# Kernel tuning notes

Hardware: AMD Instinct MI355X
Metric: run time of the kernel (lower is better)

## Reference

```python
import jax, jax.numpy as jnp
import numpy as np

IMG_H = 224
P = 3                      # roi_output_size
FEAT_HW = 13               # alexnet features[:7] spatial size for 224 input
SCALE = FEAT_HW / IMG_H
C_FEAT = 384
N_VIS = C_FEAT * P * P     # 3456
HID = 300
N_CLASSES = 4
BN_EPS = 1e-5
B, N, K2 = 8, 1024, 10     # images, total boxes, 2*context_size


def _conv(x, w, b, stride, pad):
    y = jax.lax.conv_general_dilated(x, w, (stride, stride), [(pad, pad), (pad, pad)],
                                     dimension_numbers=('NCHW', 'OIHW', 'NCHW'))
    return y + b[None, :, None, None]


def _maxpool3s2(x):
    return jax.lax.reduce_window(x, -jnp.inf, jax.lax.max, (1, 1, 3, 3), (1, 1, 2, 2), 'VALID')


def alexnet_feat(x, c1w, c1b, c2w, c2b, c3w, c3b):
    # torchvision alexnet features[:7] -> ends at conv3, NO trailing ReLU
    x = jax.nn.relu(_conv(x, c1w, c1b, 4, 2))
    x = _maxpool3s2(x)
    x = jax.nn.relu(_conv(x, c2w, c2b, 1, 2))
    x = _maxpool3s2(x)
    return _conv(x, c3w, c3b, 1, 1)


def roi_pool(feat, bboxes):
    # torchvision RoIPool: round coords by scale, per-bin max, empty bin -> 0
    H, W = feat.shape[2], feat.shape[3]
    img = bboxes[:, 0].astype(jnp.int32)
    c = jnp.round(bboxes[:, 1:] * SCALE).astype(jnp.int32)  # x1,y1,x2,y2 on feature grid
    x1, y1, x2, y2 = c[:, 0], c[:, 1], c[:, 2], c[:, 3]
    roi_w = jnp.maximum(x2 - x1 + 1, 1)
    roi_h = jnp.maximum(y2 - y1 + 1, 1)
    f = feat[img]                                   # [N,C,H,W] gather per roi
    hs = jnp.arange(H)
    ws = jnp.arange(W)
    bins = []
    for ph in range(P):
        hstart = jnp.clip(y1 + (ph * roi_h) // P, 0, H)
        hend = jnp.clip(y1 + ((ph + 1) * roi_h + P - 1) // P, 0, H)  # ceil
        mh = (hs[None, :] >= hstart[:, None]) & (hs[None, :] < hend[:, None])  # [N,H]
        for pw in range(P):
            wstart = jnp.clip(x1 + (pw * roi_w) // P, 0, W)
            wend = jnp.clip(x1 + ((pw + 1) * roi_w + P - 1) // P, 0, W)
            mw = (ws[None, :] >= wstart[:, None]) & (ws[None, :] < wend[:, None])
            mask = (mh[:, :, None] & mw[:, None, :])[:, None, :, :]  # [N,1,H,W]
            v = jnp.where(mask, f, -jnp.inf).max(axis=(2, 3))         # [N,C]
            empty = (hend <= hstart) | (wend <= wstart)
            bins.append(jnp.where(empty[:, None], 0.0, v))
    # bins ordered (ph,pw) -> [N,C,P,P], flatten like torch .view(N,-1)
    return jnp.stack(bins, axis=-1).reshape(-1, C_FEAT * P * P)


def _bn(x, g, b, m, v):
    return (x - m) * (g * jax.lax.rsqrt(v + BN_EPS)) + b


def _encoder(x, w1, b1, g, be, m, v, w2, b2):
    h = jax.nn.relu(_bn(x @ w1 + b1, g, be, m, v))  # dropout = identity (eval)
    return h @ w2 + b2


def setup_inputs() -> dict:
    key = jax.random.key(0)
    ks = jax.random.split(key, 24)
    images = jax.random.uniform(ks[0], (B, 3, IMG_H, IMG_H), jnp.float32)
    img_idx = jax.random.randint(ks[1], (N,), 0, B).astype(jnp.float32)
    xy = jax.random.uniform(ks[2], (N, 2), jnp.float32, 0.0, IMG_H - 48.0)
    wh = jax.random.uniform(ks[3], (N, 2), jnp.float32, 8.0, 48.0)
    bboxes = jnp.concatenate([img_idx[:, None], xy, xy + wh], axis=1)
    context_indices = jax.random.randint(ks[4], (N, K2), -1, N)  # -1 = padding -> zero row

    def w(k, shape, fan_in):
        return jax.random.normal(k, shape, jnp.float32) * (1.0 / np.sqrt(fan_in))

    n_total = N_VIS + HID + 4
    return {
        'images': images, 'bboxes': bboxes, 'context_indices': context_indices,
        'c1w': w(ks[5], (64, 3, 11, 11), 3 * 121), 'c1b': jnp.zeros((64,)),
        'c2w': w(ks[6], (192, 64, 5, 5), 64 * 25), 'c2b': jnp.zeros((192,)),
        'c3w': w(ks[7], (384, 192, 3, 3), 192 * 9), 'c3b': jnp.zeros((384,)),
        'enc_w1': w(ks[8], (N_VIS, HID), N_VIS), 'enc_b1': jnp.zeros((HID,)),
        'enc_g': jnp.ones((HID,)), 'enc_be': jnp.zeros((HID,)),
        'enc_m': jax.random.normal(ks[9], (HID,)) * 0.1,
        'enc_v': jax.random.uniform(ks[10], (HID,), jnp.float32, 0.5, 1.5),
        'enc_w2': w(ks[11], (HID, HID), HID), 'enc_b2': jnp.zeros((HID,)),
        'att_w': w(ks[12], (2 * HID, 1), 2 * HID), 'att_b': jnp.zeros((1,)),
        'dec_w1': w(ks[13], (n_total, n_total), n_total), 'dec_b1': jnp.zeros((n_total,)),
        'dec_g': jnp.ones((n_total,)), 'dec_be': jnp.zeros((n_total,)),
        'dec_m': jax.random.normal(ks[14], (n_total,)) * 0.1,
        'dec_v': jax.random.uniform(ks[15], (n_total,), jnp.float32, 0.5, 1.5),
        'dec_w2': w(ks[16], (n_total, N_CLASSES), n_total), 'dec_b2': jnp.zeros((N_CLASSES,)),
    }


def reference(images, bboxes, context_indices, c1w, c1b, c2w, c2b, c3w, c3b,
              enc_w1, enc_b1, enc_g, enc_be, enc_m, enc_v, enc_w2, enc_b2,
              att_w, att_b, dec_w1, dec_b1, dec_g, dec_be, dec_m, dec_v, dec_w2, dec_b2):
    n = bboxes.shape[0]
    k2 = context_indices.shape[1]
    conv_feat = alexnet_feat(images, c1w, c1b, c2w, c2b, c3w, c3b)      # [B,384,13,13]
    own = roi_pool(conv_feat, bboxes)                                   # [n, 3456]
    padded = jnp.concatenate([own, jnp.zeros((1, N_VIS), own.dtype)], 0)
    ctx = padded[context_indices.reshape(-1)].reshape(n, k2, N_VIS)     # -1 wraps to zero row

    own_enc = _encoder(own, enc_w1, enc_b1, enc_g, enc_be, enc_m, enc_v, enc_w2, enc_b2)
    ctx_enc = _encoder(ctx.reshape(n * k2, N_VIS), enc_w1, enc_b1, enc_g, enc_be,
                       enc_m, enc_v, enc_w2, enc_b2).reshape(n, k2, HID)
    # attention_layer(concat(own_enc, ctx_enc)) split into the two halves of att_w
    scores = (own_enc @ att_w[:HID, 0])[:, None] + ctx_enc @ att_w[HID:, 0] + att_b[0]  # [n,k2]
    wts = jax.nn.softmax(scores, axis=1)
    ctx_rep = jnp.einsum('nk,nkh->nh', wts, ctx_enc)                    # [n, HID]

    xywh = jnp.concatenate([bboxes[:, 1:3], bboxes[:, 3:5] - bboxes[:, 1:3]], axis=1)
    combined = jnp.concatenate([own, ctx_rep, xywh], axis=1)            # [n, 3760]
    h = jax.nn.relu(_bn(combined @ dec_w1 + dec_b1, dec_g, dec_be, dec_m, dec_v))
    return h @ dec_w2 + dec_b2                                          # [n, n_classes]
```

## Files before the change

### kernel.cpp

```cpp
#include <hip/hip_runtime.h>
#include <hip/hip_bf16.h>
#include <math.h>

#define C_FEAT 384
#define N_VIS (C_FEAT * 9)
#define HID 300
#define BN_EPS 1e-5f
#define BATCH 8
#define NROI 1024
#define K2 10
#define NTOT (N_VIS + HID + 4)
#define KPAD_DEC 3776
#define KPAD_ENC2 320

typedef _Float16 f16;
typedef f16 f16x8 __attribute__((ext_vector_type(8)));
typedef float f32x4 __attribute__((ext_vector_type(4)));
typedef int i32x4 __attribute__((ext_vector_type(4)));

__global__ void split_rowmajor(const float* __restrict__ in, f16* __restrict__ oh,
                               f16* __restrict__ ol, int R, int C, int Cpad)
{
    int idx = blockIdx.x * blockDim.x + threadIdx.x;
    if (idx >= R * Cpad) return;
    int r = idx / Cpad, c = idx % Cpad;
    float v = (c < C) ? in[(size_t)r * C + c] : 0.f;
    f16 h = (f16)v;
    oh[idx] = h;
    ol[idx] = (f16)(v - (float)h);
}

__global__ void convert_rowmajor(const float* __restrict__ in, f16* __restrict__ oh,
                                 int R, int C, int Cpad)
{
    int idx = blockIdx.x * blockDim.x + threadIdx.x;
    if (idx >= R * Cpad) return;
    int r = idx / Cpad, c = idx % Cpad;
    float v = (c < C) ? in[(size_t)r * C + c] : 0.f;
    oh[idx] = (f16)v;
}

__global__ void transpose_split(const float* __restrict__ W, int K, int Ntot, int nc0, int NC,
                                int Kpad, f16* __restrict__ Bh, f16* __restrict__ Bl)
{
    __shared__ float T[32][33];
    int k0 = blockIdx.x * 32, n0 = blockIdx.y * 32;
    int tc = threadIdx.x & 31, tr = threadIdx.x >> 5;
    #pragma unroll
    for (int i = 0; i < 4; ++i) {
        int r = tr + i * 8;
        int gk = k0 + r, nloc = n0 + tc, gn = nc0 + nloc;
        float v = 0.f;
        if (gk < K && nloc < NC && gn < Ntot) v = W[(size_t)gk * Ntot + gn];
        T[r][tc] = v;
    }
    __syncthreads();
    #pragma unroll
    for (int i = 0; i < 4; ++i) {
        int nr = tr + i * 8;
        int n = n0 + nr;
        if (n >= NC) continue;
        float v = T[tc][nr];
        f16 h = (f16)v;
        size_t o = (size_t)n * Kpad + k0 + tc;
        Bh[o] = h;
        Bl[o] = (f16)(v - (float)h);
    }
}

__global__ void transpose_convert(const float* __restrict__ W, int K, int Ntot, int nc0, int NC,
                                  int Kpad, f16* __restrict__ Bh)
{
    __shared__ float T[32][33];
    int k0 = blockIdx.x * 32, n0 = blockIdx.y * 32;
    int tc = threadIdx.x & 31, tr = threadIdx.x >> 5;
    #pragma unroll
    for (int i = 0; i < 4; ++i) {
        int r = tr + i * 8;
        int gk = k0 + r, nloc = n0 + tc, gn = nc0 + nloc;
        float v = 0.f;
        if (gk < K && nloc < NC && gn < Ntot) v = W[(size_t)gk * Ntot + gn];
        T[r][tc] = v;
    }
    __syncthreads();
    #pragma unroll
    for (int i = 0; i < 4; ++i) {
        int nr = tr + i * 8;
        int n = n0 + nr;
        if (n >= NC) continue;
        Bh[(size_t)n * Kpad + k0 + tc] = (f16)T[tc][nr];
    }
}

__global__ void im2col1_f16(const float* __restrict__ img, f16* __restrict__ ch, int b0, int nb)
{
    int idx = blockIdx.x * blockDim.x + threadIdx.x;
    int total = nb * 3025 * 384;
    if (idx >= total) return;
    int k = idx % 384, r = idx / 384;
    int ow = r % 55, t = r / 55;
    int oh = t % 55, bi = t / 55;
    float v = 0.f;
    if (k < 363) {
        int ic = k / 121, q = k % 121;
        int kh = q / 11, kw = q % 11;
        int ih = oh * 4 - 2 + kh, iw = ow * 4 - 2 + kw;
        if (ih >= 0 && ih < 224 && iw >= 0 && iw < 224)
            v = img[(((size_t)(b0 + bi) * 3 + ic) * 224 + ih) * 224 + iw];
    }
    ch[idx] = (f16)v;
}

__global__ void im2col2_f16(const float* __restrict__ in, f16* __restrict__ ch, int b0, int nb)
{
    int idx = blockIdx.x * blockDim.x + threadIdx.x;
    int total = nb * 729 * 1600;
    if (idx >= total) return;
    int k = idx % 1600, r = idx / 1600;
    int ow = r % 27, t = r / 27;
    int oh = t % 27, bi = t / 27;
    int ic = k / 25, q = k % 25;
    int kh = q / 5, kw = q % 5;
    int ih = oh - 2 + kh, iw = ow - 2 + kw;
    float v = 0.f;
    if (ih >= 0 && ih < 27 && iw >= 0 && iw < 27)
        v = in[(((size_t)(b0 + bi) * 27 + ih) * 27 + iw) * 64 + ic];
    ch[idx] = (f16)v;
}

__global__ void im2col3_f16(const float* __restrict__ in, f16* __restrict__ ch)
{
    int idx = blockIdx.x * blockDim.x + threadIdx.x;
    int total = 8 * 169 * 1728;
    if (idx >= total) return;
    int k = idx % 1728, r = idx / 1728;
    int ow = r % 13, t = r / 13;
    int oh = t % 13, bi = t / 13;
    int ic = k / 9, q = k % 9;
    int kh = q / 3, kw = q % 3;
    int ih = oh - 1 + kh, iw = ow - 1 + kw;
    float v = 0.f;
    if (ih >= 0 && ih < 13 && iw >= 0 && iw < 13)
        v = in[(((size_t)bi * 13 + ih) * 13 + iw) * 192 + ic];
    ch[idx] = (f16)v;
}

#define LDH 40
template<int TM, int TN, int BS, int MODE, int SWZ, int SPLITK, int PASSES>
__global__ __launch_bounds__(BS) void gemm_f16x3(
    const f16* __restrict__ Ah, const f16* __restrict__ Al, int lda,
    const f16* __restrict__ Bh, const f16* __restrict__ Bl, int ldb,
    float* __restrict__ C, int ldc, int M, int N, int K,
    const float* __restrict__ bias, const float* __restrict__ g,
    const float* __restrict__ be, const float* __restrict__ mean,
    const float* __restrict__ var)
{
    constexpr int NW = BS / 64;
    constexpr int WROWS = NW / 2;
    constexpr int WM = TM / (16 * WROWS);
    constexpr int WN = TN / 32;
    constexpr int AV = TM * 4 / BS;
    constexpr int BV = TN * 4 / BS;
    constexpr bool P3 = (PASSES == 3);
    __shared__ f16 sAh[TM * LDH], sBh[TN * LDH];
    __shared__ f16 sAl[(P3 ? TM : 1) * LDH], sBl[(P3 ? TN : 1) * LDH];
    int tid = threadIdx.x;
    int lane = tid & 63, w = tid >> 6;
    int wr = w >> 1, wc = w & 1;

    int bm, bn;
    if (SWZ == 2) {
        int bid = blockIdx.x;
        int x = bid & 7, l = bid >> 3;
        int mt = 2 * (x >> 1) + l / 15;
        int nt = 15 * (x & 1) + l % 15;
        bm = mt * TM; bn = nt * TN;
    } else {
        bm = blockIdx.y * TM;
        bn = blockIdx.x * TN;
    }

    int ksBeg = 0, ksEnd = K;
    if (SPLITK > 1) {
        int kc = K / SPLITK;
        ksBeg = blockIdx.z * kc;
        ksEnd = (blockIdx.z == SPLITK - 1) ? K : ksBeg + kc;
    }

    f32x4 acc[WM][WN];
    #pragma unroll
    for (int i = 0; i < WM; ++i)
        #pragma unroll
        for (int j = 0; j < WN; ++j) acc[i][j] = (f32x4){0.f, 0.f, 0.f, 0.f};

    const f16* pAh[AV]; const f16* pAl[AV]; int abase[AV]; bool avld[AV];
    #pragma unroll
    for (int i = 0; i < AV; ++i) {
        int seg = tid * AV + i;
        int row = seg >> 2, ko = (seg & 3) * 8;
        int gr = bm + row;
        avld[i] = gr < M;
        pAh[i] = Ah + (size_t)(avld[i] ? gr : 0) * lda + ko;
        if (P3) pAl[i] = Al + (size_t)(avld[i] ? gr : 0) * lda + ko;
        abase[i] = row * LDH + ko;
    }
    const f16* pBh[BV]; const f16* pBl[BV]; int bbase[BV]; bool bvld[BV];
    #pragma unroll
    for (int i = 0; i < BV; ++i) {
        int seg = tid * BV + i;
        int row = seg >> 2, ko = (seg & 3) * 8;
        int gr = bn + row;
        bvld[i] = gr < N;
        pBh[i] = Bh + (size_t)(bvld[i] ? gr : 0) * ldb + ko;
        if (P3) pBl[i] = Bl + (size_t)(bvld[i] ? gr : 0) * ldb + ko;
        bbase[i] = row * LDH + ko;
    }

    const i32x4 zz = {0, 0, 0, 0};
    i32x4 rAh[AV], rAl[AV], rBh[BV], rBl[BV];

    auto load_step = [&](int k0) {
        #pragma unroll
        for (int i = 0; i < AV; ++i) {
            rAh[i] = avld[i] ? *(const i32x4*)(pAh[i] + k0) : zz;
            if (P3) rAl[i] = avld[i] ? *(const i32x4*)(pAl[i] + k0) : zz;
        }
        #pragma unroll
        for (int i = 0; i < BV; ++i) {
            rBh[i] = bvld[i] ? *(const i32x4*)(pBh[i] + k0) : zz;
            if (P3) rBl[i] = bvld[i] ? *(const i32x4*)(pBl[i] + k0) : zz;
        }
    };
    load_step(ksBeg);

    int kfo = (lane >> 4) * 8;
    int rr = lane & 15;

    for (int k0 = ksBeg; k0 < ksEnd; k0 += 32) {
        __syncthreads();
        #pragma unroll
        for (int i = 0; i < AV; ++i) {
            *(i32x4*)&sAh[abase[i]] = rAh[i];
            if (P3) *(i32x4*)&sAl[abase[i]] = rAl[i];
        }
        #pragma unroll
        for (int i = 0; i < BV; ++i) {
            *(i32x4*)&sBh[bbase[i]] = rBh[i];
            if (P3) *(i32x4*)&sBl[bbase[i]] = rBl[i];
        }
        __syncthreads();
        if (k0 + 32 < ksEnd) load_step(k0 + 32);

        f16x8 fah[WM], fal[WM], fbh[WN], fbl[WN];
        #pragma unroll
        for (int m = 0; m < WM; ++m) {
            int row = wr * (WM * 16) + m * 16 + rr;
            fah[m] = *(const f16x8*)&sAh[row * LDH + kfo];
            if (P3) fal[m] = *(const f16x8*)&sAl[row * LDH + kfo];
        }
        #pragma unroll
        for (int n = 0; n < WN; ++n) {
            int row = wc * (WN * 16) + n * 16 + rr;
            fbh[n] = *(const f16x8*)&sBh[row * LDH + kfo];
            if (P3) fbl[n] = *(const f16x8*)&sBl[row * LDH + kfo];
        }
        #pragma unroll
        for (int m = 0; m < WM; ++m)
            #pragma unroll
            for (int n = 0; n < WN; ++n) {
                acc[m][n] = __builtin_amdgcn_mfma_f32_16x16x32_f16(fah[m], fbh[n], acc[m][n], 0, 0, 0);
                if (P3) {
                    acc[m][n] = __builtin_amdgcn_mfma_f32_16x16x32_f16(fah[m], fbl[n], acc[m][n], 0, 0, 0);
                    acc[m][n] = __builtin_amdgcn_mfma_f32_16x16x32_f16(fal[m], fbh[n], acc[m][n], 0, 0, 0);
                }
            }
    }

    int crl = lane >> 4;
    size_t zoff = (SPLITK > 1) ? (size_t)blockIdx.z * M : 0;
    #pragma unroll
    for (int m = 0; m < WM; ++m) {
        #pragma unroll
        for (int n = 0; n < WN; ++n) {
            int gn = bn + wc * (WN * 16) + n * 16 + rr;
            if (gn >= N) continue;
            #pragma unroll
            for (int r = 0; r < 4; ++r) {
                int gm = bm + wr * (WM * 16) + m * 16 + crl * 4 + r;
                if (gm >= M) continue;
                if (SPLITK > 1) {
                    C[(zoff + gm) * ldc + gn] = acc[m][n][r];
                } else {
                    float v = acc[m][n][r] + bias[gn];
                    if (MODE == 1) {
                        float s = g[gn] / sqrtf(var[gn] + BN_EPS);
                        v = (v - mean[gn]) * s + be[gn];
                        v = fmaxf(v, 0.f);
                    } else if (MODE == 2) {
                        v = fmaxf(v, 0.f);
                    }
                    C[(size_t)gm * ldc + gn] = v;
                }
            }
        }
    }
}

template<int MODE>
__global__ void reduce_ep(const float* __restrict__ part, float* __restrict__ C,
                          int M, int N, int ldc, int KS,
                          const float* __restrict__ bias, const float* __restrict__ g,
                          const float* __restrict__ be, const float* __restrict__ mean,
                          const float* __restrict__ var)
{
    int idx = blockIdx.x * blockDim.x + threadIdx.x;
    if (idx >= M * N) return;
    int m = idx / N, n = idx % N;
    float v = 0.f;
    for (int ks = 0; ks < KS; ++ks) v += part[((size_t)ks * M + m) * N + n];
    v += bias[n];
    if (MODE == 1) {
        float s = g[n] / sqrtf(var[n] + BN_EPS);
        v = (v - mean[n]) * s + be[n];
        v = fmaxf(v, 0.f);
    } else if (MODE == 2) {
        v = fmaxf(v, 0.f);
    }
    C[(size_t)m * ldc + n] = v;
}

__global__ void maxpool3s2_nhwc(const float* __restrict__ in, float* __restrict__ out,
                                int Bn, int C, int Hin, int Win, int Hout, int Wout)
{
    int idx = blockIdx.x * blockDim.x + threadIdx.x;
    int total = Bn * Hout * Wout * C;
    if (idx >= total) return;
    int c = idx % C, t = idx / C;
    int ow = t % Wout; t /= Wout;
    int oh = t % Hout; int b = t / Hout;
    const float* base = in + (((size_t)b * Hin + oh * 2) * Win + ow * 2) * C + c;
    float v = -INFINITY;
    #pragma unroll
    for (int kh = 0; kh < 3; ++kh)
        #pragma unroll
        for (int kw = 0; kw < 3; ++kw)
            v = fmaxf(v, base[((size_t)kh * Win + kw) * C]);
    out[idx] = v;
}

__global__ void roi_pool_kernel(const float* __restrict__ feat, const float* __restrict__ bboxes,
                                float* __restrict__ own, int N, int C, int H, int W)
{
    int idx = blockIdx.x * blockDim.x + threadIdx.x;
    if (idx >= N * C) return;
    int n = idx / C, c = idx % C;
    const float* bb = bboxes + (size_t)n * 5;
    int img = (int)bb[0];
    const float SC = 13.0f / 224.0f;
    int x1 = (int)rintf(bb[1] * SC);
    int y1 = (int)rintf(bb[2] * SC);
    int x2 = (int)rintf(bb[3] * SC);
    int y2 = (int)rintf(bb[4] * SC);
    int roi_w = max(x2 - x1 + 1, 1);
    int roi_h = max(y2 - y1 + 1, 1);
    const float* f = feat + (size_t)img * H * W * C + c;
    float* o = own + (size_t)n * (C * 9) + (size_t)c * 9;
    for (int ph = 0; ph < 3; ++ph) {
        int hstart = min(max(y1 + (ph * roi_h) / 3, 0), H);
        int hend   = min(max(y1 + ((ph + 1) * roi_h + 2) / 3, 0), H);
        for (int pw = 0; pw < 3; ++pw) {
            int wstart = min(max(x1 + (pw * roi_w) / 3, 0), W);
            int wend   = min(max(x1 + ((pw + 1) * roi_w + 2) / 3, 0), W);
            float v;
            if (hend <= hstart || wend <= wstart) {
                v = 0.f;
            } else {
                v = -INFINITY;
                for (int hh = hstart; hh < hend; ++hh)
                    for (int ww = wstart; ww < wend; ++ww)
                        v = fmaxf(v, f[((size_t)hh * W + ww) * C]);
            }
            o[ph * 3 + pw] = v;
        }
    }
}

__global__ void zero_kernel(float* __restrict__ p, int n)
{
    int i = blockIdx.x * blockDim.x + threadIdx.x;
    if (i < n) p[i] = 0.f;
}

__global__ __launch_bounds__(128) void proj_kernel(
    const float* __restrict__ enc_all, const float* __restrict__ att_w,
    float* __restrict__ s_own, float* __restrict__ proj_hi, int R, int H, int Nroi)
{
    int r = blockIdx.x, tid = threadIdx.x;
    const float* row = enc_all + (size_t)r * H;
    float plo = 0.f, phi = 0.f;
    for (int hh = tid; hh < H; hh += 128) {
        float v = row[hh];
        plo += v * att_w[hh];
        phi += v * att_w[H + hh];
    }
    __shared__ float slo[128], shi[128];
    slo[tid] = plo; shi[tid] = phi;
    __syncthreads();
    for (int s = 64; s > 0; s >>= 1) {
        if (tid < s) { slo[tid] += slo[tid + s]; shi[tid] += shi[tid + s]; }
        __syncthreads();
    }
    if (tid == 0) {
        if (r < Nroi) s_own[r] = slo[0];
        proj_hi[r] = shi[0];
    }
}

__global__ __launch_bounds__(512) void att_combine_kernel(
    const float* __restrict__ enc_all, const int* __restrict__ ci,
    const float* __restrict__ s_own, const float* __restrict__ proj_hi,
    const float* __restrict__ att_b, const float* __restrict__ own,
    const float* __restrict__ bboxes, float* __restrict__ combined,
    int N, int H)
{
    int n = blockIdx.x, tid = threadIdx.x;
    __shared__ float wts[K2];
    __shared__ int rows[K2];
    if (tid < K2) {
        int idx = ci[(size_t)n * K2 + tid];
        int row = (idx < 0) ? N : idx;
        rows[tid] = row;
        wts[tid] = s_own[n] + proj_hi[row] + att_b[0];
    }
    __syncthreads();
    if (tid == 0) {
        float mx = wts[0];
        #pragma unroll
        for (int k = 1; k < K2; ++k) mx = fmaxf(mx, wts[k]);
        float sum = 0.f;
        float e[K2];
        #pragma unroll
        for (int k = 0; k < K2; ++k) { e[k] = expf(wts[k] - mx); sum += e[k]; }
        float inv = 1.f / sum;
        #pragma unroll
        for (int k = 0; k < K2; ++k) wts[k] = e[k] * inv;
    }
    __syncthreads();

    float* crow = combined + (size_t)n * NTOT;
    if (tid < H) {
        float acc = 0.f;
        #pragma unroll
        for (int k = 0; k < K2; ++k)
            acc += wts[k] * enc_all[(size_t)rows[k] * H + tid];
        crow[N_VIS + tid] = acc;
    }
    const float* orow = own + (size_t)n * N_VIS;
    for (int j = tid; j < N_VIS; j += 512) crow[j] = orow[j];
    if (tid >= 508) {
        int j = tid - 508;
        float x1 = bboxes[(size_t)n * 5 + 1];
        float y1 = bboxes[(size_t)n * 5 + 2];
        float x2 = bboxes[(size_t)n * 5 + 3];
        float y2 = bboxes[(size_t)n * 5 + 4];
        float vals[4] = { x1, y1, x2 - x1, y2 - y1 };
        crow[N_VIS + HID + j] = vals[j];
    }
}

__global__ __launch_bounds__(256) void gemv4_kernel(
    const float* __restrict__ h, const float* __restrict__ w2,
    const float* __restrict__ b2, float* __restrict__ out, int K)
{
    int m = blockIdx.x, tid = threadIdx.x;
    const float* hr = h + (size_t)m * K;
    float a0 = 0.f, a1 = 0.f, a2 = 0.f, a3 = 0.f;
    for (int k = tid; k < K; k += 256) {
        float x = hr[k];
        const float* wr = w2 + (size_t)k * 4;
        a0 += x * wr[0]; a1 += x * wr[1]; a2 += x * wr[2]; a3 += x * wr[3];
    }
    __shared__ float red[256][4];
    red[tid][0] = a0; red[tid][1] = a1; red[tid][2] = a2; red[tid][3] = a3;
    __syncthreads();
    for (int s = 128; s > 0; s >>= 1) {
        if (tid < s) {
            #pragma unroll
            for (int j = 0; j < 4; ++j) red[tid][j] += red[tid + s][j];
        }
        __syncthreads();
    }
    if (tid < 4) out[(size_t)m * 4 + tid] = red[0][tid] + b2[tid];
}

extern "C" void kernel_launch(void* const* d_in, const int* in_sizes, int n_in,
                              void* d_out, int out_size, void* d_ws, size_t ws_size,
                              hipStream_t stream)
{
    const float* images = (const float*)d_in[0];
    const float* bboxes = (const float*)d_in[1];
    const int*   ci     = (const int*)  d_in[2];
    const float* c1w = (const float*)d_in[3];
    const float* c1b = (const float*)d_in[4];
    const float* c2w = (const float*)d_in[5];
    const float* c2b = (const float*)d_in[6];
    const float* c3w = (const float*)d_in[7];
    const float* c3b = (const float*)d_in[8];
    const float* enc_w1 = (const float*)d_in[9];
    const float* enc_b1 = (const float*)d_in[10];
    const float* enc_g  = (const float*)d_in[11];
    const float* enc_be = (const float*)d_in[12];
    const float* enc_m  = (const float*)d_in[13];
    const float* enc_v  = (const float*)d_in[14];
    const float* enc_w2 = (const float*)d_in[15];
    const float* enc_b2 = (const float*)d_in[16];
    const float* att_w  = (const float*)d_in[17];
    const float* att_b  = (const float*)d_in[18];
    const float* dec_w1 = (const float*)d_in[19];
    const float* dec_b1 = (const float*)d_in[20];
    const float* dec_g  = (const float*)d_in[21];
    const float* dec_be = (const float*)d_in[22];
    const float* dec_m  = (const float*)d_in[23];
    const float* dec_v  = (const float*)d_in[24];
    const float* dec_w2 = (const float*)d_in[25];
    const float* dec_b2 = (const float*)d_in[26];
    float* out = (float*)d_out;

    float* ws = (float*)d_ws;
    size_t off = 0;
    auto alloc = [&](size_t n) { float* p = ws + off; off += (n + 255) & ~(size_t)255; return p; };

    float* own      = alloc((size_t)(NROI + 1) * N_VIS);
    float* featN    = alloc((size_t)BATCH * 13 * 13 * C_FEAT);
    float* mid      = alloc((size_t)(NROI + 1) * HID);
    float* enc_all  = alloc((size_t)(NROI + 1) * HID);
    float* s_own    = alloc(NROI);
    float* proj_hi  = alloc(NROI + 1);
    float* combined = alloc((size_t)NROI * NTOT);
    float* hbuf     = alloc((size_t)NROI * NTOT);
    size_t base_off = off;

    const size_t BTD_FL = 7128320;
    bool full_dec = (ws_size >= (base_off + 2 * BTD_FL) * sizeof(float));
    float* Btd_h_f = ws + base_off;
    float* Btd_l_f = ws + base_off + BTD_FL;

    float* S = combined;

    f16* wt1_h = (f16*)(S + 6651904);
    f16* wt2_h = wt1_h + 24576;
    f16* wt3_h = wt2_h + 307200;

    convert_rowmajor<<<(64 * 384 + 255) / 256, 256, 0, stream>>>(c1w, wt1_h, 64, 363, 384);
    convert_rowmajor<<<(192 * 1600 + 255) / 256, 256, 0, stream>>>(c2w, wt2_h, 192, 1600, 1600);
    convert_rowmajor<<<(384 * 1728 + 255) / 256, 256, 0, stream>>>(c3w, wt3_h, 384, 1728, 1728);

    float* conv1o = S;
    float* pool1  = S + 1548800;
    float* conv2o = S;

    if (full_dec) {
        f16* colF = (f16*)Btd_h_f;
        float* part2 = S + 1922048;
        float* pool2 = S + 4161536;
        float* part3 = S;

        {
            int total = 8 * 3025 * 384;
            im2col1_f16<<<(total + 255) / 256, 256, 0, stream>>>(images, colF, 0, 8);
            dim3 grid(1, (8 * 3025 + 63) / 64);
            gemm_f16x3<64, 64, 256, 2, 0, 1, 1><<<grid, 256, 0, stream>>>(
                colF, nullptr, 384, wt1_h, nullptr, 384,
                conv1o, 64, 8 * 3025, 64, 384,
                c1b, nullptr, nullptr, nullptr, nullptr);
        }
        maxpool3s2_nhwc<<<(BATCH * 27 * 27 * 64 + 255) / 256, 256, 0, stream>>>(
            conv1o, pool1, BATCH, 64, 55, 55, 27, 27);

        {
            int total = 8 * 729 * 1600;
            im2col2_f16<<<(total + 255) / 256, 256, 0, stream>>>(pool1, colF, 0, 8);
            dim3 grid(3, (8 * 729 + 63) / 64, 2);
            gemm_f16x3<64, 64, 256, 0, 0, 2, 1><<<grid, 256, 0, stream>>>(
                colF, nullptr, 1600, wt2_h, nullptr, 1600,
                part2, 192, 8 * 729, 192, 1600,
                nullptr, nullptr, nullptr, nullptr, nullptr);
            reduce_ep<2><<<(8 * 729 * 192 + 255) / 256, 256, 0, stream>>>(
                part2, conv2o, 8 * 729, 192, 192, 2, c2b, nullptr, nullptr, nullptr, nullptr);
        }
        maxpool3s2_nhwc<<<(BATCH * 13 * 13 * 192 + 255) / 256, 256, 0, stream>>>(
            conv2o, pool2, BATCH, 192, 27, 27, 13, 13);

        {
            int total = 8 * 169 * 1728;
            im2col3_f16<<<(total + 255) / 256, 256, 0, stream>>>(pool2, colF);
            dim3 grid(6, (8 * 169 + 63) / 64, 2);
            gemm_f16x3<64, 64, 256, 0, 0, 2, 1><<<grid, 256, 0, stream>>>(
                colF, nullptr, 1728, wt3_h, nullptr, 1728,
                part3, 384, 8 * 169, 384, 1728,
                nullptr, nullptr, nullptr, nullptr, nullptr);
            reduce_ep<0><<<(8 * 169 * 384 + 255) / 256, 256, 0, stream>>>(
                part3, featN, 8 * 169, 384, 384, 2, c3b, nullptr, nullptr, nullptr, nullptr);
        }
    } else {
        f16* col_h = (f16*)(S + 1922048);
        float* pool2 = S + 1548800;
        for (int ch = 0; ch < 2; ++ch) {
            int b0 = ch * 4, nb = 4;
            int total = nb * 3025 * 384;
            im2col1_f16<<<(total + 255) / 256, 256, 0, stream>>>(images, col_h, b0, nb);
            dim3 grid(1, (nb * 3025 + 63) / 64);
            gemm_f16x3<64, 64, 256, 2, 0, 1, 1><<<grid, 256, 0, stream>>>(
                col_h, nullptr, 384, wt1_h, nullptr, 384,
                conv1o + (size_t)b0 * 3025 * 64, 64, nb * 3025, 64, 384,
                c1b, nullptr, nullptr, nullptr, nullptr);
        }
        maxpool3s2_nhwc<<<(BATCH * 27 * 27 * 64 + 255) / 256, 256, 0, stream>>>(
            conv1o, pool1, BATCH, 64, 55, 55, 27, 27);
        for (int ch = 0; ch < 2; ++ch) {
            int b0 = ch * 4, nb = 4;
            int total = nb * 729 * 1600;
            im2col2_f16<<<(total + 255) / 256, 256, 0, stream>>>(pool1, col_h, b0, nb);
            dim3 grid(3, (nb * 729 + 63) / 64);
            gemm_f16x3<64, 64, 256, 2, 0, 1, 1><<<grid, 256, 0, stream>>>(
                col_h, nullptr, 1600, wt2_h, nullptr, 1600,
                conv2o + (size_t)b0 * 729 * 192, 192, nb * 729, 192, 1600,
                c2b, nullptr, nullptr, nullptr, nullptr);
        }
        maxpool3s2_nhwc<<<(BATCH * 13 * 13 * 192 + 255) / 256, 256, 0, stream>>>(
            conv2o, pool2, BATCH, 192, 27, 27, 13, 13);
        {
            int total = 8 * 169 * 1728;
            im2col3_f16<<<(total + 255) / 256, 256, 0, stream>>>(pool2, col_h);
            dim3 grid(6, (8 * 169 + 63) / 64);
            gemm_f16x3<64, 64, 256, 0, 0, 1, 1><<<grid, 256, 0, stream>>>(
                col_h, nullptr, 1728, wt3_h, nullptr, 1728,
                featN, 384, 8 * 169, 384, 1728,
                c3b, nullptr, nullptr, nullptr, nullptr);
        }
    }

    roi_pool_kernel<<<(NROI * C_FEAT + 255) / 256, 256, 0, stream>>>(featN, bboxes, own, NROI, C_FEAT, 13, 13);
    zero_kernel<<<(N_VIS + 255) / 256, 256, 0, stream>>>(own + (size_t)NROI * N_VIS, N_VIS);

    f16* own_h  = (f16*)(S + 0);
    f16* encB_h = (f16*)(S + 1771200);
    convert_rowmajor<<<((NROI + 1) * N_VIS + 255) / 256, 256, 0, stream>>>(
        own, own_h, NROI + 1, N_VIS, N_VIS);
    {
        dim3 tg((N_VIS + 31) / 32, (HID + 31) / 32);
        transpose_convert<<<tg, 256, 0, stream>>>(enc_w1, N_VIS, HID, 0, HID, N_VIS, encB_h);
    }
    if (full_dec) {
        float* part1 = S + 2289600;
        dim3 grid((HID + 63) / 64, (NROI + 1 + 63) / 64, 4);
        gemm_f16x3<64, 64, 256, 0, 0, 4, 1><<<grid, 256, 0, stream>>>(
            own_h, nullptr, N_VIS, encB_h, nullptr, N_VIS,
            part1, HID, NROI + 1, HID, N_VIS,
            nullptr, nullptr, nullptr, nullptr, nullptr);
        reduce_ep<1><<<((NROI + 1) * HID + 255) / 256, 256, 0, stream>>>(
            part1, mid, NROI + 1, HID, HID, 4, enc_b1, enc_g, enc_be, enc_m, enc_v);
    } else {
        dim3 grid((HID + 63) / 64, (NROI + 1 + 63) / 64);
        gemm_f16x3<64, 64, 256, 1, 0, 1, 1><<<grid, 256, 0, stream>>>(
            own_h, nullptr, N_VIS, encB_h, nullptr, N_VIS,
            mid, HID, NROI + 1, HID, N_VIS,
            enc_b1, enc_g, enc_be, enc_m, enc_v);
    }

    f16* mid_h = (f16*)(S + 3519600);
    f16* e2B_h = (f16*)(S + 3683600);
    convert_rowmajor<<<((NROI + 1) * KPAD_ENC2 + 255) / 256, 256, 0, stream>>>(
        mid, mid_h, NROI + 1, HID, KPAD_ENC2);
    {
        dim3 tg((HID + 31) / 32, (HID + 31) / 32);
        transpose_convert<<<tg, 256, 0, stream>>>(enc_w2, HID, HID, 0, HID, KPAD_ENC2, e2B_h);
    }
    {
        dim3 grid((HID + 63) / 64, (NROI + 1 + 63) / 64);
        gemm_f16x3<64, 64, 256, 0, 0, 1, 1><<<grid, 256, 0, stream>>>(
            mid_h, nullptr, KPAD_ENC2, e2B_h, nullptr, KPAD_ENC2,
            enc_all, HID, NROI + 1, HID, KPAD_ENC2,
            enc_b2, nullptr, nullptr, nullptr, nullptr);
    }

    proj_kernel<<<NROI + 1, 128, 0, stream>>>(enc_all, att_w, s_own, proj_hi, NROI + 1, HID, NROI);
    att_combine_kernel<<<NROI, 512, 0, stream>>>(enc_all, ci, s_own, proj_hi, att_b,
                                                 own, bboxes, combined, NROI, HID);

    f16* comb_h = (f16*)own;
    f16* comb_l = (f16*)(own + 1933312);
    split_rowmajor<<<(NROI * KPAD_DEC + 255) / 256, 256, 0, stream>>>(
        combined, comb_h, comb_l, NROI, NTOT, KPAD_DEC);

    if (full_dec) {
        f16* Btd_h = (f16*)Btd_h_f;
        f16* Btd_l = (f16*)Btd_l_f;
        dim3 tg(KPAD_DEC / 32, KPAD_DEC / 32);
        transpose_split<<<tg, 256, 0, stream>>>(dec_w1, NTOT, NTOT, 0, KPAD_DEC, KPAD_DEC, Btd_h, Btd_l);
        float* part = combined;
        dim3 grid(240, 1, 2);
        gemm_f16x3<128, 128, 512, 1, 2, 2, 3><<<grid, 512, 0, stream>>>(
            comb_h, comb_l, KPAD_DEC, Btd_h, Btd_l, KPAD_DEC,
            part, NTOT, NROI, NTOT, KPAD_DEC,
            nullptr, nullptr, nullptr, nullptr, nullptr);
        reduce_ep<1><<<(NROI * NTOT + 255) / 256, 256, 0, stream>>>(
            part, hbuf, NROI, NTOT, NTOT, 2, dec_b1, dec_g, dec_be, dec_m, dec_v);
    } else {
        f16* Btc_h = (f16*)(S + 0);
        f16* Btc_l = (f16*)(S + 1774720);
        for (int c = 0; c < 4; ++c) {
            int nc0 = c * 940, NC = 940;
            dim3 tg(KPAD_DEC / 32, (NC + 31) / 32);
            transpose_split<<<tg, 256, 0, stream>>>(dec_w1, NTOT, NTOT, nc0, NC, KPAD_DEC, Btc_h, Btc_l);
            dim3 grid((NC + 63) / 64, NROI / 64);
            gemm_f16x3<64, 64, 256, 1, 0, 1, 3><<<grid, 256, 0, stream>>>(
                comb_h, comb_l, KPAD_DEC, Btc_h, Btc_l, KPAD_DEC,
                hbuf + nc0, NTOT, NROI, NC, KPAD_DEC,
                dec_b1 + nc0, dec_g + nc0, dec_be + nc0, dec_m + nc0, dec_v + nc0);
        }
    }

    gemv4_kernel<<<NROI, 256, 0, stream>>>(hbuf, dec_w2, dec_b2, out, NTOT);
}
```

Baseline: 338.0 us.

## Double-buffer GEMM register prefetch, fuse f16 RoI output and decoder epilogue

```diff
diff --git a/kernel.cpp b/kernel.cpp
--- a/kernel.cpp
+++ b/kernel.cpp
@@ -217,40 +217,62 @@
     }
 
     const i32x4 zz = {0, 0, 0, 0};
-    i32x4 rAh[AV], rAl[AV], rBh[BV], rBl[BV];
-
-    auto load_step = [&](int k0) {
+    i32x4 rAh0[AV], rAl0[AV], rBh0[BV], rBl0[BV];
+    i32x4 rAh1[AV], rAl1[AV], rBh1[BV], rBl1[BV];
+
+    auto load0 = [&](int k0) {
         #pragma unroll
         for (int i = 0; i < AV; ++i) {
-            rAh[i] = avld[i] ? *(const i32x4*)(pAh[i] + k0) : zz;
-            if (P3) rAl[i] = avld[i] ? *(const i32x4*)(pAl[i] + k0) : zz;
+            rAh0[i] = avld[i] ? *(const i32x4*)(pAh[i] + k0) : zz;
+            if (P3) rAl0[i] = avld[i] ? *(const i32x4*)(pAl[i] + k0) : zz;
         }
         #pragma unroll
         for (int i = 0; i < BV; ++i) {
-            rBh[i] = bvld[i] ? *(const i32x4*)(pBh[i] + k0) : zz;
-            if (P3) rBl[i] = bvld[i] ? *(const i32x4*)(pBl[i] + k0) : zz;
+            rBh0[i] = bvld[i] ? *(const i32x4*)(pBh[i] + k0) : zz;
+            if (P3) rBl0[i] = bvld[i] ? *(const i32x4*)(pBl[i] + k0) : zz;
         }
     };
-    load_step(ksBeg);
+    auto load1 = [&](int k0) {
+        #pragma unroll
+        for (int i = 0; i < AV; ++i) {
+            rAh1[i] = avld[i] ? *(const i32x4*)(pAh[i] + k0) : zz;
+            if (P3) rAl1[i] = avld[i] ? *(const i32x4*)(pAl[i] + k0) : zz;
+        }
+        #pragma unroll
+        for (int i = 0; i < BV; ++i) {
+            rBh1[i] = bvld[i] ? *(const i32x4*)(pBh[i] + k0) : zz;
+            if (P3) rBl1[i] = bvld[i] ? *(const i32x4*)(pBl[i] + k0) : zz;
+        }
+    };
+    auto stage0 = [&]() {
+        #pragma unroll
+        for (int i = 0; i < AV; ++i) {
+            *(i32x4*)&sAh[abase[i]] = rAh0[i];
+            if (P3) *(i32x4*)&sAl[abase[i]] = rAl0[i];
+        }
+        #pragma unroll
+        for (int i = 0; i < BV; ++i) {
+            *(i32x4*)&sBh[bbase[i]] = rBh0[i];
+            if (P3) *(i32x4*)&sBl[bbase[i]] = rBl0[i];
+        }
+    };
+    auto stage1 = [&]() {
+        #pragma unroll
+        for (int i = 0; i < AV; ++i) {
+            *(i32x4*)&sAh[abase[i]] = rAh1[i];
+            if (P3) *(i32x4*)&sAl[abase[i]] = rAl1[i];
+        }
+        #pragma unroll
+        for (int i = 0; i < BV; ++i) {
+            *(i32x4*)&sBh[bbase[i]] = rBh1[i];
+            if (P3) *(i32x4*)&sBl[bbase[i]] = rBl1[i];
+        }
+    };
 
     int kfo = (lane >> 4) * 8;
     int rr = lane & 15;
 
-    for (int k0 = ksBeg; k0 < ksEnd; k0 += 32) {
-        __syncthreads();
-        #pragma unroll
-        for (int i = 0; i < AV; ++i) {
-            *(i32x4*)&sAh[abase[i]] = rAh[i];
-            if (P3) *(i32x4*)&sAl[abase[i]] = rAl[i];
-        }
-        #pragma unroll
-        for (int i = 0; i < BV; ++i) {
-            *(i32x4*)&sBh[bbase[i]] = rBh[i];
-            if (P3) *(i32x4*)&sBl[bbase[i]] = rBl[i];
-        }
-        __syncthreads();
-        if (k0 + 32 < ksEnd) load_step(k0 + 32);
-
+    auto compute = [&]() {
         f16x8 fah[WM], fal[WM], fbh[WN], fbl[WN];
         #pragma unroll
         for (int m = 0; m < WM; ++m) {
@@ -274,6 +296,24 @@
                     acc[m][n] = __builtin_amdgcn_mfma_f32_16x16x32_f16(fal[m], fbh[n], acc[m][n], 0, 0, 0);
                 }
             }
+    };
+
+    load0(ksBeg);
+    if (ksBeg + 32 < ksEnd) load1(ksBeg + 32);
+
+    for (int k0 = ksBeg; k0 < ksEnd; k0 += 64) {
+        __syncthreads();
+        stage0();
+        __syncthreads();
+        if (k0 + 64 < ksEnd) load0(k0 + 64);
+        compute();
+        if (k0 + 32 < ksEnd) {
+            __syncthreads();
+            stage1();
+            __syncthreads();
+            if (k0 + 96 < ksEnd) load1(k0 + 96);
+            compute();
+        }
     }
 
     int crl = lane >> 4;
@@ -349,7 +389,8 @@
 }
 
 __global__ void roi_pool_kernel(const float* __restrict__ feat, const float* __restrict__ bboxes,
-                                float* __restrict__ own, int N, int C, int H, int W)
+                                float* __restrict__ own, f16* __restrict__ own_h,
+                                int N, int C, int H, int W)
 {
     int idx = blockIdx.x * blockDim.x + threadIdx.x;
     if (idx >= N * C) return;
@@ -365,6 +406,7 @@
     int roi_h = max(y2 - y1 + 1, 1);
     const float* f = feat + (size_t)img * H * W * C + c;
     float* o = own + (size_t)n * (C * 9) + (size_t)c * 9;
+    f16* oh16 = own_h + (size_t)n * (C * 9) + (size_t)c * 9;
     for (int ph = 0; ph < 3; ++ph) {
         int hstart = min(max(y1 + (ph * roi_h) / 3, 0), H);
         int hend   = min(max(y1 + ((ph + 1) * roi_h + 2) / 3, 0), H);
@@ -381,6 +423,7 @@
                         v = fmaxf(v, f[((size_t)hh * W + ww) * C]);
             }
             o[ph * 3 + pw] = v;
+            oh16[ph * 3 + pw] = (f16)v;
         }
     }
 }
@@ -389,6 +432,12 @@
 {
     int i = blockIdx.x * blockDim.x + threadIdx.x;
     if (i < n) p[i] = 0.f;
+}
+
+__global__ void zero16_kernel(f16* __restrict__ p, int n)
+{
+    int i = blockIdx.x * blockDim.x + threadIdx.x;
+    if (i < n) p[i] = (f16)0.f;
 }
 
 __global__ __launch_bounds__(128) void proj_kernel(
@@ -479,6 +528,38 @@
         float x = hr[k];
         const float* wr = w2 + (size_t)k * 4;
         a0 += x * wr[0]; a1 += x * wr[1]; a2 += x * wr[2]; a3 += x * wr[3];
+    }
+    __shared__ float red[256][4];
+    red[tid][0] = a0; red[tid][1] = a1; red[tid][2] = a2; red[tid][3] = a3;
+    __syncthreads();
+    for (int s = 128; s > 0; s >>= 1) {
+        if (tid < s) {
+            #pragma unroll
+            for (int j = 0; j < 4; ++j) red[tid][j] += red[tid + s][j];
+        }
+        __syncthreads();
+    }
+    if (tid < 4) out[(size_t)m * 4 + tid] = red[0][tid] + b2[tid];
+}
+
+__global__ __launch_bounds__(256) void gemv4_fused_kernel(
+    const float* __restrict__ part, const float* __restrict__ w2,
+    const float* __restrict__ b2, const float* __restrict__ bias,
+    const float* __restrict__ g, const float* __restrict__ be,
+    const float* __restrict__ mean, const float* __restrict__ var,
+    float* __restrict__ out, int M, int K)
+{
+    int m = blockIdx.x, tid = threadIdx.x;
+    const float* p0 = part + (size_t)m * K;
+    const float* p1 = part + ((size_t)M + m) * K;
+    float a0 = 0.f, a1 = 0.f, a2 = 0.f, a3 = 0.f;
+    for (int k = tid; k < K; k += 256) {
+        float v = p0[k] + p1[k] + bias[k];
+        float s = g[k] / sqrtf(var[k] + BN_EPS);
+        v = (v - mean[k]) * s + be[k];
+        v = fmaxf(v, 0.f);
+        const float* wr = w2 + (size_t)k * 4;
+        a0 += v * wr[0]; a1 += v * wr[1]; a2 += v * wr[2]; a3 += v * wr[3];
     }
     __shared__ float red[256][4];
     red[tid][0] = a0; red[tid][1] = a1; red[tid][2] = a2; red[tid][3] = a3;
@@ -640,13 +721,13 @@
         }
     }
 
-    roi_pool_kernel<<<(NROI * C_FEAT + 255) / 256, 256, 0, stream>>>(featN, bboxes, own, NROI, C_FEAT, 13, 13);
+    f16* own_h = (f16*)(S + 0);
+    roi_pool_kernel<<<(NROI * C_FEAT + 255) / 256, 256, 0, stream>>>(
+        featN, bboxes, own, own_h, NROI, C_FEAT, 13, 13);
     zero_kernel<<<(N_VIS + 255) / 256, 256, 0, stream>>>(own + (size_t)NROI * N_VIS, N_VIS);
-
-    f16* own_h  = (f16*)(S + 0);
+    zero16_kernel<<<(N_VIS + 255) / 256, 256, 0, stream>>>(own_h + (size_t)NROI * N_VIS, N_VIS);
+
     f16* encB_h = (f16*)(S + 1771200);
-    convert_rowmajor<<<((NROI + 1) * N_VIS + 255) / 256, 256, 0, stream>>>(
-        own, own_h, NROI + 1, N_VIS, N_VIS);
     {
         dim3 tg((N_VIS + 31) / 32, (HID + 31) / 32);
         transpose_convert<<<tg, 256, 0, stream>>>(enc_w1, N_VIS, HID, 0, HID, N_VIS, encB_h);
@@ -704,8 +785,9 @@
             comb_h, comb_l, KPAD_DEC, Btd_h, Btd_l, KPAD_DEC,
             part, NTOT, NROI, NTOT, KPAD_DEC,
             nullptr, nullptr, nullptr, nullptr, nullptr);
-        reduce_ep<1><<<(NROI * NTOT + 255) / 256, 256, 0, stream>>>(
-            part, hbuf, NROI, NTOT, NTOT, 2, dec_b1, dec_g, dec_be, dec_m, dec_v);
+        gemv4_fused_kernel<<<NROI, 256, 0, stream>>>(
+            part, dec_w2, dec_b2, dec_b1, dec_g, dec_be, dec_m, dec_v,
+            out, NROI, NTOT);
     } else {
         f16* Btc_h = (f16*)(S + 0);
         f16* Btc_l = (f16*)(S + 1774720);
@@ -719,7 +801,6 @@
                 hbuf + nc0, NTOT, NROI, NC, KPAD_DEC,
                 dec_b1 + nc0, dec_g + nc0, dec_be + nc0, dec_m + nc0, dec_v + nc0);
         }
-    }
-
-    gemv4_kernel<<<NROI, 256, 0, stream>>>(hbuf, dec_w2, dec_b2, out, NTOT);
-}
+        gemv4_kernel<<<NROI, 256, 0, stream>>>(hbuf, dec_w2, dec_b2, out, NTOT);
+    }
+}
```

New measurement: 358.3 us. 1.06x slower.
